# Kernel tuning notes

Measured on AMD Instinct MI355X. Metric: run time of the kernel, lower is better.

## Reference

```python
import jax, jax.numpy as jnp
import numpy as np

B, DIM = 16384, 1024
H1, H2, H3 = 500, 200, 200


def setup_inputs() -> dict:
    key = jax.random.key(0)
    ks = jax.random.split(key, 16)
    s = 0.01
    return {
        "x": jax.random.normal(ks[0], (B, DIM), dtype=jnp.float32),
        "show_index": jax.random.randint(ks[1], (B,), 0, 100),
        "st": jax.random.normal(ks[2], (1000, 16), dtype=jnp.float32),
        # deep MLP params (shared across the two task heads, as in the source)
        "W1": jax.random.normal(ks[3], (DIM, H1), dtype=jnp.float32) * s,
        "b1": jnp.zeros((H1,), dtype=jnp.float32),
        "W2": jax.random.normal(ks[4], (H1, H2), dtype=jnp.float32) * s,
        "b2": jnp.zeros((H2,), dtype=jnp.float32),
        "W3": jax.random.normal(ks[5], (H2, H3), dtype=jnp.float32) * s,
        "b3": jnp.zeros((H3,), dtype=jnp.float32),
        # final sigmoid head on concat([emb(DIM), d3(H3)])
        "Wl": jax.random.normal(ks[6], (DIM + H3, 1), dtype=jnp.float32) * s,
        "bl": jnp.zeros((1,), dtype=jnp.float32),
        # per-(task, cross-layer) cross weights/biases: tf.random_normal stddev=0.01
        "cw": jax.random.normal(ks[7], (2, 3, DIM), dtype=jnp.float32) * s,
        "cb": jax.random.normal(ks[8], (2, 3, DIM), dtype=jnp.float32) * s,
    }


def reference(x, show_index, st, W1, b1, W2, b2, W3, b3, Wl, bl, cw, cb):
    # Deep part (same shared Dense layers each task -> compute once).
    d = jax.nn.relu(x @ W1 + b1)
    d = jax.nn.relu(d @ W2 + b2)
    d3 = jax.nn.relu(d @ W3 + b3)  # (B, H3)

    # cross_net: sum_i w[j] * x[b,i] * emb[b,j]  ==  x.sum(1) * emb[b,j] * w[j]
    # (collapsed form of the (B,dim,dim) outer product + axis-1 reduction)
    xsum = jnp.sum(x, axis=1, keepdims=True)  # (B, 1)
    preds = []
    for i in range(2):
        emb = x
        for j in range(3):
            emb = xsum * emb * cw[i, j] + cb[i, j] + x
        mid = jnp.concatenate([emb, d3], axis=-1)  # (B, DIM+H3)
        preds.append(jax.nn.sigmoid(mid @ Wl + bl))  # (B, 1)
    return tuple(preds)
```

## Files before the change

### kernel.cpp

```cpp
#include <hip/hip_runtime.h>
#include <hip/hip_bf16.h>
#include <math.h>

#define B_ROWS 16384
#define DIM 1024

typedef __attribute__((ext_vector_type(8))) short s16x8;
typedef __attribute__((ext_vector_type(4))) float f32x4;

static __device__ __forceinline__ unsigned short f2bf(float f) {
    union { float f; unsigned u; } v; v.f = f;
    unsigned r = v.u + 0x7FFF + ((v.u >> 16) & 1);
    return (unsigned short)(r >> 16);
}

static __device__ __forceinline__ void gload16(const unsigned short* g, unsigned short* l) {
    __builtin_amdgcn_global_load_lds(
        (const __attribute__((address_space(1))) unsigned int*)g,
        (__attribute__((address_space(3))) unsigned int*)l, 16, 0, 0);
}

__global__ __launch_bounds__(256) void prep(
    const float* __restrict__ x, unsigned short* __restrict__ xb,
    const float* __restrict__ W1, const float* __restrict__ W2,
    const float* __restrict__ W3,
    const float* __restrict__ cw, const float* __restrict__ cb,
    const float* __restrict__ Wl,
    unsigned short* __restrict__ W1b, unsigned short* __restrict__ W2b,
    unsigned short* __restrict__ W3b,
    float* __restrict__ czz) {
    __shared__ unsigned short tile[64][72];
    __shared__ float red[4][6];
    const int tid = threadIdx.x;
    const int blk = blockIdx.x;

    if (blk < 4096) {
        const float* src = x + (size_t)blk * 4096;
        unsigned short* dst = xb + (size_t)blk * 4096;
#pragma unroll
        for (int r = 0; r < 4; ++r) {
            float4 f = *(const float4*)(src + r * 1024 + tid * 4);
            short4 h;
            h.x = (short)f2bf(f.x); h.y = (short)f2bf(f.y);
            h.z = (short)f2bf(f.z); h.w = (short)f2bf(f.w);
            *(short4*)(dst + r * 1024 + tid * 4) = h;
        }
    } else if (blk < 4272) {
        const int w = blk - 4096;
        const float* src; unsigned short* dst;
        int kt, nt, Ksrc, Nsrc, ldDst;
        bool skipHi = false;
        if (w < 128)      { kt = w & 15;         nt = w >> 4;         src = W1; dst = W1b; Ksrc = 1024; Nsrc = 500; ldDst = 1024; skipHi = true; }
        else if (w < 160) { kt = (w - 128) & 7;  nt = (w - 128) >> 3; src = W2; dst = W2b; Ksrc = 500;  Nsrc = 200; ldDst = 512;  }
        else              { kt = (w - 160) & 3;  nt = (w - 160) >> 2; src = W3; dst = W3b; Ksrc = 200;  Nsrc = 200; ldDst = 256;  }
        const int k0 = kt << 6, n0 = nt << 6;
        {
            const int r = tid >> 2, c0 = (tid & 3) << 4;
            const int kk = k0 + r;
#pragma unroll
            for (int i = 0; i < 16; ++i) {
                const int nn = n0 + c0 + i;
                const float v = (kk < Ksrc && nn < Nsrc) ? src[(size_t)kk * Nsrc + nn] : 0.f;
                tile[r][c0 + i] = f2bf(v);
            }
        }
        __syncthreads();
        {
            const int n = tid >> 2, kc = (tid & 3) << 4;
            if (!(skipHi && (n0 + n) >= 500)) {
                unsigned short* o = dst + (size_t)(n0 + n) * ldDst + k0 + kc;
#pragma unroll
                for (int i = 0; i < 16; ++i) o[i] = tile[kc + i][n];
            }
        }
    } else if (blk == 4272) {
#pragma unroll
        for (int q = 0; q < 4; ++q) {
            const int k = tid * 4 + q;
            const float wl = Wl[k];
            const float a1 = cw[k],         a2 = cw[1024 + k],  a3 = cw[2048 + k];
            const float d1_ = cw[3072 + k], d2_ = cw[4096 + k], d3_ = cw[5120 + k];
            W1b[(size_t)500 * 1024 + k] = f2bf(a1 * a2 * a3 * wl);
            W1b[(size_t)501 * 1024 + k] = f2bf(a2 * a3 * wl);
            W1b[(size_t)502 * 1024 + k] = f2bf(a3 * wl);
            W1b[(size_t)503 * 1024 + k] = f2bf(d1_ * d2_ * d3_ * wl);
            W1b[(size_t)504 * 1024 + k] = f2bf(d2_ * d3_ * wl);
            W1b[(size_t)505 * 1024 + k] = f2bf(d3_ * wl);
            W1b[(size_t)506 * 1024 + k] = f2bf(wl);
            W1b[(size_t)507 * 1024 + k] = 0x3F80;
            W1b[(size_t)508 * 1024 + k] = 0;
            W1b[(size_t)509 * 1024 + k] = 0;
            W1b[(size_t)510 * 1024 + k] = 0;
            W1b[(size_t)511 * 1024 + k] = 0;
        }
    } else {
        float c[6] = {0.f, 0.f, 0.f, 0.f, 0.f, 0.f};
#pragma unroll
        for (int q = 0; q < 4; ++q) {
            const int k = tid * 4 + q;
            const float wl = Wl[k];
            {
                const float w2 = cw[1024 + k], w3 = cw[2048 + k];
                const float b1 = cb[k], b2 = cb[1024 + k], b3 = cb[2048 + k];
                c[0] += w2 * w3 * b1 * wl;
                c[1] += w3 * b2 * wl;
                c[2] += b3 * wl;
            }
            {
                const float w2 = cw[4096 + k], w3 = cw[5120 + k];
                const float b1 = cb[3072 + k], b2 = cb[4096 + k], b3 = cb[5120 + k];
                c[3] += w2 * w3 * b1 * wl;
                c[4] += w3 * b2 * wl;
                c[5] += b3 * wl;
            }
        }
        const int lane = tid & 63, wv = tid >> 6;
#pragma unroll
        for (int j = 0; j < 6; ++j)
#pragma unroll
            for (int m = 1; m < 64; m <<= 1) c[j] += __shfl_xor(c[j], m, 64);
        if (lane == 0)
#pragma unroll
            for (int j = 0; j < 6; ++j) red[wv][j] = c[j];
        __syncthreads();
        if (tid < 6) czz[tid] = red[0][tid] + red[1][tid] + red[2][tid] + red[3][tid];
    }
}

template <int ROWS>
static __device__ __forceinline__ void stage_tile(
    const unsigned short* __restrict__ src, int K, int rowBase, int kt,
    unsigned short* lds, int w, int lane) {
    const int r8   = lane >> 3;
    const int slot = lane & 7;
#pragma unroll
    for (int q = 0; q < ROWS / 32; ++q) {
        const int blk   = q * 4 + w;
        const int row   = blk * 8 + r8;
        const int chunk = slot ^ (row & 7);
        const unsigned short* g = src + (size_t)(rowBase + row) * K + kt * 64 + chunk * 8;
        gload16(g, lds + blk * 512);
    }
}

template <int ROWS>
static __device__ __forceinline__ void stage8(
    const unsigned short* __restrict__ src, int K, int rowBase, int kt,
    unsigned short* lds, int w, int lane) {
    const int r8   = lane >> 3;
    const int slot = lane & 7;
#pragma unroll
    for (int q = 0; q < ROWS / 64; ++q) {
        const int blk   = q * 8 + w;
        const int row   = blk * 8 + r8;
        const int chunk = slot ^ (row & 7);
        const unsigned short* g = src + (size_t)(rowBase + row) * K + kt * 64 + chunk * 8;
        gload16(g, lds + blk * 512);
    }
}

__global__ __launch_bounds__(256) void gemm_bf16(
    const unsigned short* __restrict__ A,
    const unsigned short* __restrict__ Bw,
    const float* __restrict__ bias,
    unsigned short* __restrict__ C,
    float* __restrict__ zparts) {
    constexpr int K = 1024, ldc = 512, BM = 128, nK = 16;
    __shared__ unsigned short As[2][BM * 64];
    __shared__ unsigned short Bs[2][128 * 64];

    const int tid  = threadIdx.x;
    const int lane = tid & 63;
    const int wid  = tid >> 6;
    const int wm   = wid >> 1;
    const int wn   = wid & 1;
    const int g    = lane >> 4;
    const int r16  = lane & 15;

    const int cpx = gridDim.x >> 3;
    const int swz = (blockIdx.x & 7) * cpx + (blockIdx.x >> 3);
    const int rowBase = (swz >> 2) * BM;
    const int colBase = (swz & 3) << 7;

    f32x4 acc[4][4];
#pragma unroll
    for (int m = 0; m < 4; ++m)
#pragma unroll
        for (int n = 0; n < 4; ++n)
            acc[m][n] = (f32x4){0.f, 0.f, 0.f, 0.f};

    stage_tile<BM>(A, K, rowBase, 0, As[0], wid, lane);
    stage_tile<128>(Bw, K, colBase, 0, Bs[0], wid, lane);
    asm volatile("s_waitcnt vmcnt(0)" ::: "memory");
    __builtin_amdgcn_s_barrier();
    asm volatile("" ::: "memory");

    for (int kt = 0; kt < nK; ++kt) {
        const int buf = kt & 1;
        if (kt + 1 < nK) {
            stage_tile<BM>(A, K, rowBase, kt + 1, As[buf ^ 1], wid, lane);
            stage_tile<128>(Bw, K, colBase, kt + 1, Bs[buf ^ 1], wid, lane);
        }
        asm volatile("" ::: "memory");

        const unsigned short* Ab = As[buf];
        const unsigned short* Bb = Bs[buf];
#pragma unroll
        for (int ks = 0; ks < 2; ++ks) {
            s16x8 af[4], bfr[4];
#pragma unroll
            for (int m = 0; m < 4; ++m) {
                const int row = wm * 64 + m * 16 + r16;
                const int off = ((ks * 4 + g) * 16) ^ ((row & 7) << 4);
                af[m] = *(const s16x8*)((const char*)Ab + row * 128 + off);
            }
#pragma unroll
            for (int n = 0; n < 4; ++n) {
                const int row = wn * 64 + n * 16 + r16;
                const int off = ((ks * 4 + g) * 16) ^ ((row & 7) << 4);
                bfr[n] = *(const s16x8*)((const char*)Bb + row * 128 + off);
            }
#pragma unroll
            for (int m = 0; m < 4; ++m)
#pragma unroll
                for (int n = 0; n < 4; ++n)
                    acc[m][n] = __builtin_amdgcn_mfma_f32_16x16x32_bf16(af[m], bfr[n], acc[m][n], 0, 0, 0);
        }

        if (kt + 1 < nK)
            asm volatile("s_waitcnt vmcnt(0)" ::: "memory");
        __builtin_amdgcn_s_barrier();
        asm volatile("" ::: "memory");
    }

    unsigned short* Cb = As[0];
#pragma unroll
    for (int n = 0; n < 4; ++n) {
        const int col = colBase + wn * 64 + n * 16 + r16;
        const int lcol = wn * 64 + n * 16 + r16;
        const float bv = (col < 500) ? bias[col] : 0.f;
        const unsigned pc = (unsigned)(col - 500);
#pragma unroll
        for (int m = 0; m < 4; ++m) {
            const int lrow = wm * 64 + m * 16 + g * 4;
#pragma unroll
            for (int r = 0; r < 4; ++r) {
                const float raw = acc[m][n][r];
                if (pc < 8u) zparts[(size_t)(rowBase + lrow + r) * 8 + pc] = raw;
                float v = raw + bv;
                v = v > 0.f ? v : 0.f;
                Cb[(lrow + r) * 128 + lcol] = f2bf(v);
            }
        }
    }
    __syncthreads();

    {
        const int row  = tid >> 1;
        const int half = tid & 1;
        const uint4* s = (const uint4*)(Cb + row * 128 + half * 64);
        uint4* d = (uint4*)(C + (size_t)(rowBase + row) * ldc + colBase + half * 64);
        d[0] = s[0];
        d[1] = s[1];
        d[2] = s[2];
        d[3] = s[3];
    }
}

__global__ __launch_bounds__(512) void tail_fused(
    const unsigned short* __restrict__ d1,
    const unsigned short* __restrict__ W2b,
    const float* __restrict__ b2,
    const unsigned short* __restrict__ W3b,
    const float* __restrict__ b3,
    const float* __restrict__ Wl,
    const float* __restrict__ bl,
    const float* __restrict__ zparts,
    const float* __restrict__ czz,
    float* __restrict__ out) {
    __shared__ unsigned short As[2][64 * 64];
    __shared__ unsigned short Bs[2][256 * 64];
    __shared__ unsigned short P[64 * 256];
    __shared__ float part[8][64];

    const int tid  = threadIdx.x;
    const int lane = tid & 63;
    const int wid  = tid >> 6;
    const int wm   = wid >> 2;
    const int wn   = wid & 3;
    const int g    = lane >> 4;
    const int r16  = lane & 15;
    const int rowBase = blockIdx.x << 6;

    f32x4 acc[2][4];
#pragma unroll
    for (int m = 0; m < 2; ++m)
#pragma unroll
        for (int n = 0; n < 4; ++n)
            acc[m][n] = (f32x4){0.f, 0.f, 0.f, 0.f};

    stage8<64>(d1, 512, rowBase, 0, As[0], wid, lane);
    stage8<256>(W2b, 512, 0, 0, Bs[0], wid, lane);

    for (int kt = 0; kt < 8; ++kt) {
        const int buf = kt & 1;
        if (kt + 1 < 8) {
            stage8<64>(d1, 512, rowBase, kt + 1, As[buf ^ 1], wid, lane);
            stage8<256>(W2b, 512, 0, kt + 1, Bs[buf ^ 1], wid, lane);
            asm volatile("s_waitcnt vmcnt(5)" ::: "memory");
        } else {
            asm volatile("s_waitcnt vmcnt(0)" ::: "memory");
        }
        __builtin_amdgcn_s_barrier();
        asm volatile("" ::: "memory");

        const unsigned short* Ab = As[buf];
        const unsigned short* Bb = Bs[buf];
#pragma unroll
        for (int ks = 0; ks < 2; ++ks) {
            s16x8 af[2], bfr[4];
#pragma unroll
            for (int m = 0; m < 2; ++m) {
                const int row = wm * 32 + m * 16 + r16;
                const int off = ((ks * 4 + g) * 16) ^ ((row & 7) << 4);
                af[m] = *(const s16x8*)((const char*)Ab + row * 128 + off);
            }
#pragma unroll
            for (int n = 0; n < 4; ++n) {
                const int row = wn * 64 + n * 16 + r16;
                const int off = ((ks * 4 + g) * 16) ^ ((row & 7) << 4);
                bfr[n] = *(const s16x8*)((const char*)Bb + row * 128 + off);
            }
#pragma unroll
            for (int m = 0; m < 2; ++m)
#pragma unroll
                for (int n = 0; n < 4; ++n)
                    acc[m][n] = __builtin_amdgcn_mfma_f32_16x16x32_bf16(af[m], bfr[n], acc[m][n], 0, 0, 0);
        }
        asm volatile("s_waitcnt lgkmcnt(0)" ::: "memory");
        __builtin_amdgcn_s_barrier();
        asm volatile("" ::: "memory");
    }

#pragma unroll
    for (int n = 0; n < 4; ++n) {
        const int col = wn * 64 + n * 16 + r16;
        const float bv = (col < 200) ? b2[col] : 0.f;
#pragma unroll
        for (int m = 0; m < 2; ++m) {
#pragma unroll
            for (int r = 0; r < 4; ++r) {
                const int row = wm * 32 + m * 16 + g * 4 + r;
                float v = acc[m][n][r] + bv;
                v = v > 0.f ? v : 0.f;
                const int byte = row * 512 + ((col * 2) ^ ((row & 7) << 4));
                *(unsigned short*)((char*)P + byte) = f2bf(v);
            }
        }
    }

    stage8<256>(W3b, 256, 0, 0, Bs[0], wid, lane);
    asm volatile("s_waitcnt lgkmcnt(0)" ::: "memory");
    __builtin_amdgcn_s_barrier();
    asm volatile("" ::: "memory");

    f32x4 acc2[2][4];
#pragma unroll
    for (int m = 0; m < 2; ++m)
#pragma unroll
        for (int n = 0; n < 4; ++n)
            acc2[m][n] = (f32x4){0.f, 0.f, 0.f, 0.f};

    for (int kt = 0; kt < 4; ++kt) {
        const int buf = kt & 1;
        if (kt + 1 < 4) {
            stage8<256>(W3b, 256, 0, kt + 1, Bs[buf ^ 1], wid, lane);
            asm volatile("s_waitcnt vmcnt(4)" ::: "memory");
        } else {
            asm volatile("s_waitcnt vmcnt(0)" ::: "memory");
        }
        __builtin_amdgcn_s_barrier();
        asm volatile("" ::: "memory");

        const unsigned short* Bb = Bs[buf];
#pragma unroll
        for (int ks = 0; ks < 2; ++ks) {
            s16x8 af[2], bfr[4];
#pragma unroll
            for (int m = 0; m < 2; ++m) {
                const int row = wm * 32 + m * 16 + r16;
                const int byte = row * 512 + ((kt * 128 + (ks * 4 + g) * 16) ^ ((row & 7) << 4));
                af[m] = *(const s16x8*)((const char*)P + byte);
            }
#pragma unroll
            for (int n = 0; n < 4; ++n) {
                const int row = wn * 64 + n * 16 + r16;
                const int off = ((ks * 4 + g) * 16) ^ ((row & 7) << 4);
                bfr[n] = *(const s16x8*)((const char*)Bb + row * 128 + off);
            }
#pragma unroll
            for (int m = 0; m < 2; ++m)
#pragma unroll
                for (int n = 0; n < 4; ++n)
                    acc2[m][n] = __builtin_amdgcn_mfma_f32_16x16x32_bf16(af[m], bfr[n], acc2[m][n], 0, 0, 0);
        }
        asm volatile("s_waitcnt lgkmcnt(0)" ::: "memory");
        __builtin_amdgcn_s_barrier();
        asm volatile("" ::: "memory");
    }

    float wlv[4], b3v[4];
#pragma unroll
    for (int n = 0; n < 4; ++n) {
        const int col = wn * 64 + n * 16 + r16;
        wlv[n] = (col < 200) ? Wl[1024 + col] : 0.f;
        b3v[n] = (col < 200) ? b3[col] : 0.f;
    }
#pragma unroll
    for (int m = 0; m < 2; ++m) {
#pragma unroll
        for (int r = 0; r < 4; ++r) {
            float s = 0.f;
#pragma unroll
            for (int n = 0; n < 4; ++n) {
                float v = acc2[m][n][r] + b3v[n];
                v = v > 0.f ? v : 0.f;
                s += v * wlv[n];
            }
            s += __shfl_xor(s, 1, 64);
            s += __shfl_xor(s, 2, 64);
            s += __shfl_xor(s, 4, 64);
            s += __shfl_xor(s, 8, 64);
            if (r16 == 0) part[wid][wm * 32 + m * 16 + g * 4 + r] = s;
        }
    }
    __syncthreads();

    if (tid < 64) {
        const int row = rowBase + tid;
        const int wmr = (tid >> 5) << 2;
        const float t = part[wmr][tid] + part[wmr + 1][tid] +
                        part[wmr + 2][tid] + part[wmr + 3][tid];
        const float blv = bl[0];
        const float* zp = zparts + (size_t)row * 8;
        float4 zpa = *(const float4*)(zp);
        float4 zpb = *(const float4*)(zp + 4);
        const float s = zpb.w;
        const float z0 = ((zpa.x * s + zpa.y + czz[0]) * s + zpa.z + czz[1]) * s
                         + zpb.z + czz[2] + t + blv;
        const float z1 = ((zpa.w * s + zpb.x + czz[3]) * s + zpb.y + czz[4]) * s
                         + zpb.z + czz[5] + t + blv;
        out[row]          = 1.f / (1.f + expf(-z0));
        out[B_ROWS + row] = 1.f / (1.f + expf(-z1));
    }
}

extern "C" void kernel_launch(void* const* d_in, const int* in_sizes, int n_in,
                              void* d_out, int out_size, void* d_ws, size_t ws_size,
                              hipStream_t stream) {
    const float* x  = (const float*)d_in[0];
    const float* W1 = (const float*)d_in[3];
    const float* b1 = (const float*)d_in[4];
    const float* W2 = (const float*)d_in[5];
    const float* b2 = (const float*)d_in[6];
    const float* W3 = (const float*)d_in[7];
    const float* b3 = (const float*)d_in[8];
    const float* Wl = (const float*)d_in[9];
    const float* bl = (const float*)d_in[10];
    const float* cw = (const float*)d_in[11];
    const float* cb = (const float*)d_in[12];
    float* out = (float*)d_out;

    unsigned short* xb  = (unsigned short*)d_ws;
    unsigned short* d1  = xb + (size_t)16384 * 1024;
    unsigned short* W1b = d1 + (size_t)16384 * 512;
    unsigned short* W2b = W1b + (size_t)512 * 1024;
    unsigned short* W3b = W2b + (size_t)256 * 512;
    float* zparts = (float*)(W3b + (size_t)256 * 256);
    float* czz = zparts + (size_t)16384 * 8;

    prep<<<4274, 256, 0, stream>>>(x, xb, W1, W2, W3, cw, cb, Wl,
                                   W1b, W2b, W3b, czz);

    gemm_bf16<<<512, 256, 0, stream>>>(xb, W1b, b1, d1, zparts);

    tail_fused<<<256, 512, 0, stream>>>(d1, W2b, b2, W3b, b3, Wl, bl,
                                        zparts, czz, out);
}
```

Measured before the change: 61.46 us.

## Switch first-layer GEMM to FP8 and compute cross-net dot products in FP32

Quantizes x and W1 to FP8 (E4M3, with W1 scaled by 64) and runs the first GEMM with FP8 MFMA instructions over 128-byte K tiles. The cross-net per-row dot products move from extra W1 rows inside the GEMM to a separate FP32 kernel, which also writes the FP8 copy of x. The goal is to halve GEMM operand bytes and raise MFMA throughput. The cost is lower precision in the deep path and one extra kernel launch.

```diff
diff --git a/kernel.cpp b/kernel.cpp
--- a/kernel.cpp
+++ b/kernel.cpp
@@ -14,45 +14,44 @@
     return (unsigned short)(r >> 16);
 }
 
-static __device__ __forceinline__ void gload16(const unsigned short* g, unsigned short* l) {
+static __device__ __forceinline__ unsigned f2fp8(float f) {
+    union { float f; unsigned u; } v; v.f = f;
+    const unsigned s = (v.u >> 24) & 0x80u;
+    const float a = fabsf(f);
+    if (a >= 448.f) return s | 0x7Eu;
+    if (a < 0.015625f) {
+        const int q = (int)rintf(a * 512.f);
+        return s | (unsigned)q;
+    }
+    unsigned b = v.u & 0x7fffffffu;
+    b += 0x000FFFFFu + ((b >> 20) & 1u);
+    const int e = (int)(b >> 23) - 127;
+    const unsigned m = (b >> 20) & 7u;
+    return s | (unsigned)((e + 7) << 3) | m;
+}
+
+static __device__ __forceinline__ void gload16(const void* g, void* l) {
     __builtin_amdgcn_global_load_lds(
         (const __attribute__((address_space(1))) unsigned int*)g,
         (__attribute__((address_space(3))) unsigned int*)l, 16, 0, 0);
 }
 
-__global__ __launch_bounds__(256) void prep(
-    const float* __restrict__ x, unsigned short* __restrict__ xb,
+__global__ __launch_bounds__(256) void prep_w(
     const float* __restrict__ W1, const float* __restrict__ W2,
     const float* __restrict__ W3,
     const float* __restrict__ cw, const float* __restrict__ cb,
     const float* __restrict__ Wl,
-    unsigned short* __restrict__ W1b, unsigned short* __restrict__ W2b,
-    unsigned short* __restrict__ W3b,
+    unsigned char* __restrict__ W1q,
+    unsigned short* __restrict__ W2b, unsigned short* __restrict__ W3b,
     float* __restrict__ czz) {
     __shared__ unsigned short tile[64][72];
+    __shared__ unsigned char tilec[64][72];
     __shared__ float red[4][6];
     const int tid = threadIdx.x;
     const int blk = blockIdx.x;
 
-    if (blk < 4096) {
-        const float* src = x + (size_t)blk * 4096;
-        unsigned short* dst = xb + (size_t)blk * 4096;
-#pragma unroll
-        for (int r = 0; r < 4; ++r) {
-            float4 f = *(const float4*)(src + r * 1024 + tid * 4);
-            short4 h;
-            h.x = (short)f2bf(f.x); h.y = (short)f2bf(f.y);
-            h.z = (short)f2bf(f.z); h.w = (short)f2bf(f.w);
-            *(short4*)(dst + r * 1024 + tid * 4) = h;
-        }
-    } else if (blk < 4272) {
-        const int w = blk - 4096;
-        const float* src; unsigned short* dst;
-        int kt, nt, Ksrc, Nsrc, ldDst;
-        bool skipHi = false;
-        if (w < 128)      { kt = w & 15;         nt = w >> 4;         src = W1; dst = W1b; Ksrc = 1024; Nsrc = 500; ldDst = 1024; skipHi = true; }
-        else if (w < 160) { kt = (w - 128) & 7;  nt = (w - 128) >> 3; src = W2; dst = W2b; Ksrc = 500;  Nsrc = 200; ldDst = 512;  }
-        else              { kt = (w - 160) & 3;  nt = (w - 160) >> 2; src = W3; dst = W3b; Ksrc = 200;  Nsrc = 200; ldDst = 256;  }
+    if (blk < 128) {
+        const int kt = blk & 15, nt = blk >> 4;
         const int k0 = kt << 6, n0 = nt << 6;
         {
             const int r = tid >> 2, c0 = (tid & 3) << 4;
@@ -60,38 +59,40 @@
 #pragma unroll
             for (int i = 0; i < 16; ++i) {
                 const int nn = n0 + c0 + i;
-                const float v = (kk < Ksrc && nn < Nsrc) ? src[(size_t)kk * Nsrc + nn] : 0.f;
-                tile[r][c0 + i] = f2bf(v);
+                const float v = (nn < 500) ? W1[(size_t)kk * 500 + nn] * 64.f : 0.f;
+                tilec[r][c0 + i] = (unsigned char)f2fp8(v);
             }
         }
         __syncthreads();
         {
             const int n = tid >> 2, kc = (tid & 3) << 4;
-            if (!(skipHi && (n0 + n) >= 500)) {
-                unsigned short* o = dst + (size_t)(n0 + n) * ldDst + k0 + kc;
-#pragma unroll
-                for (int i = 0; i < 16; ++i) o[i] = tile[kc + i][n];
-            }
-        }
-    } else if (blk == 4272) {
-#pragma unroll
-        for (int q = 0; q < 4; ++q) {
-            const int k = tid * 4 + q;
-            const float wl = Wl[k];
-            const float a1 = cw[k],         a2 = cw[1024 + k],  a3 = cw[2048 + k];
-            const float d1_ = cw[3072 + k], d2_ = cw[4096 + k], d3_ = cw[5120 + k];
-            W1b[(size_t)500 * 1024 + k] = f2bf(a1 * a2 * a3 * wl);
-            W1b[(size_t)501 * 1024 + k] = f2bf(a2 * a3 * wl);
-            W1b[(size_t)502 * 1024 + k] = f2bf(a3 * wl);
-            W1b[(size_t)503 * 1024 + k] = f2bf(d1_ * d2_ * d3_ * wl);
-            W1b[(size_t)504 * 1024 + k] = f2bf(d2_ * d3_ * wl);
-            W1b[(size_t)505 * 1024 + k] = f2bf(d3_ * wl);
-            W1b[(size_t)506 * 1024 + k] = f2bf(wl);
-            W1b[(size_t)507 * 1024 + k] = 0x3F80;
-            W1b[(size_t)508 * 1024 + k] = 0;
-            W1b[(size_t)509 * 1024 + k] = 0;
-            W1b[(size_t)510 * 1024 + k] = 0;
-            W1b[(size_t)511 * 1024 + k] = 0;
+            unsigned char* o = W1q + (size_t)(n0 + n) * 1024 + k0 + kc;
+#pragma unroll
+            for (int i = 0; i < 16; ++i) o[i] = tilec[kc + i][n];
+        }
+    } else if (blk < 176) {
+        const int w = blk;
+        const float* src; unsigned short* dst;
+        int kt, nt, Ksrc, Nsrc, ldDst;
+        if (w < 160) { kt = (w - 128) & 7;  nt = (w - 128) >> 3; src = W2; dst = W2b; Ksrc = 500; Nsrc = 200; ldDst = 512; }
+        else         { kt = (w - 160) & 3;  nt = (w - 160) >> 2; src = W3; dst = W3b; Ksrc = 200; Nsrc = 200; ldDst = 256; }
+        const int k0 = kt << 6, n0 = nt << 6;
+        {
+            const int r = tid >> 2, c0 = (tid & 3) << 4;
+            const int kk = k0 + r;
+#pragma unroll
+            for (int i = 0; i < 16; ++i) {
+                const int nn = n0 + c0 + i;
+                const float v = (kk < Ksrc && nn < Nsrc) ? src[(size_t)kk * Nsrc + nn] : 0.f;
+                tile[r][c0 + i] = f2bf(v);
+            }
+        }
+        __syncthreads();
+        {
+            const int n = tid >> 2, kc = (tid & 3) << 4;
+            unsigned short* o = dst + (size_t)(n0 + n) * ldDst + k0 + kc;
+#pragma unroll
+            for (int i = 0; i < 16; ++i) o[i] = tile[kc + i][n];
         }
     } else {
         float c[6] = {0.f, 0.f, 0.f, 0.f, 0.f, 0.f};
@@ -127,47 +128,97 @@
     }
 }
 
-template <int ROWS>
-static __device__ __forceinline__ void stage_tile(
-    const unsigned short* __restrict__ src, int K, int rowBase, int kt,
-    unsigned short* lds, int w, int lane) {
+__global__ __launch_bounds__(256) void xdots(
+    const float* __restrict__ x,
+    const float* __restrict__ cw, const float* __restrict__ Wl,
+    unsigned char* __restrict__ xq,
+    float* __restrict__ zparts) {
+    const int tid  = threadIdx.x;
+    const int lane = tid & 63;
+    const int w    = tid >> 6;
+    const int row0 = (blockIdx.x << 4) + (w << 2);
+
+    float d[4][8];
+#pragma unroll
+    for (int r = 0; r < 4; ++r)
+#pragma unroll
+        for (int j = 0; j < 8; ++j) d[r][j] = 0.f;
+
+#pragma unroll
+    for (int c = 0; c < 4; ++c) {
+        const int kb = c * 256 + lane * 4;
+        const float4 wl4 = *(const float4*)(Wl + kb);
+        const float4 c0 = *(const float4*)(cw + kb);
+        const float4 c1 = *(const float4*)(cw + 1024 + kb);
+        const float4 c2 = *(const float4*)(cw + 2048 + kb);
+        const float4 c3 = *(const float4*)(cw + 3072 + kb);
+        const float4 c4 = *(const float4*)(cw + 4096 + kb);
+        const float4 c5 = *(const float4*)(cw + 5120 + kb);
+        float4 p10, p20, p30, p11, p21, p31;
+        p10.x = c2.x * wl4.x; p10.y = c2.y * wl4.y; p10.z = c2.z * wl4.z; p10.w = c2.w * wl4.w;
+        p20.x = c1.x * p10.x; p20.y = c1.y * p10.y; p20.z = c1.z * p10.z; p20.w = c1.w * p10.w;
+        p30.x = c0.x * p20.x; p30.y = c0.y * p20.y; p30.z = c0.z * p20.z; p30.w = c0.w * p20.w;
+        p11.x = c5.x * wl4.x; p11.y = c5.y * wl4.y; p11.z = c5.z * wl4.z; p11.w = c5.w * wl4.w;
+        p21.x = c4.x * p11.x; p21.y = c4.y * p11.y; p21.z = c4.z * p11.z; p21.w = c4.w * p11.w;
+        p31.x = c3.x * p21.x; p31.y = c3.y * p21.y; p31.z = c3.z * p21.z; p31.w = c3.w * p21.w;
+
+#pragma unroll
+        for (int r = 0; r < 4; ++r) {
+            const float4 xv = *(const float4*)(x + (size_t)(row0 + r) * DIM + kb);
+            d[r][0] += xv.x * p30.x + xv.y * p30.y + xv.z * p30.z + xv.w * p30.w;
+            d[r][1] += xv.x * p20.x + xv.y * p20.y + xv.z * p20.z + xv.w * p20.w;
+            d[r][2] += xv.x * p10.x + xv.y * p10.y + xv.z * p10.z + xv.w * p10.w;
+            d[r][3] += xv.x * p31.x + xv.y * p31.y + xv.z * p31.z + xv.w * p31.w;
+            d[r][4] += xv.x * p21.x + xv.y * p21.y + xv.z * p21.z + xv.w * p21.w;
+            d[r][5] += xv.x * p11.x + xv.y * p11.y + xv.z * p11.z + xv.w * p11.w;
+            d[r][6] += xv.x * wl4.x + xv.y * wl4.y + xv.z * wl4.z + xv.w * wl4.w;
+            d[r][7] += xv.x + xv.y + xv.z + xv.w;
+            const unsigned u = f2fp8(xv.x) | (f2fp8(xv.y) << 8) |
+                               (f2fp8(xv.z) << 16) | (f2fp8(xv.w) << 24);
+            *(unsigned*)(xq + (size_t)(row0 + r) * DIM + kb) = u;
+        }
+    }
+
+#pragma unroll
+    for (int r = 0; r < 4; ++r)
+#pragma unroll
+        for (int j = 0; j < 8; ++j)
+#pragma unroll
+            for (int m = 1; m < 64; m <<= 1)
+                d[r][j] += __shfl_xor(d[r][j], m, 64);
+
+    if (lane == 0) {
+#pragma unroll
+        for (int r = 0; r < 4; ++r)
+#pragma unroll
+            for (int j = 0; j < 8; ++j)
+                zparts[(size_t)(row0 + r) * 8 + j] = d[r][j];
+    }
+}
+
+static __device__ __forceinline__ void stage_fp8(
+    const unsigned char* __restrict__ src, int rowBase, int kt,
+    unsigned char* lds, int w, int lane) {
     const int r8   = lane >> 3;
     const int slot = lane & 7;
 #pragma unroll
-    for (int q = 0; q < ROWS / 32; ++q) {
+    for (int q = 0; q < 4; ++q) {
         const int blk   = q * 4 + w;
         const int row   = blk * 8 + r8;
         const int chunk = slot ^ (row & 7);
-        const unsigned short* g = src + (size_t)(rowBase + row) * K + kt * 64 + chunk * 8;
-        gload16(g, lds + blk * 512);
-    }
-}
-
-template <int ROWS>
-static __device__ __forceinline__ void stage8(
-    const unsigned short* __restrict__ src, int K, int rowBase, int kt,
-    unsigned short* lds, int w, int lane) {
-    const int r8   = lane >> 3;
-    const int slot = lane & 7;
-#pragma unroll
-    for (int q = 0; q < ROWS / 64; ++q) {
-        const int blk   = q * 8 + w;
-        const int row   = blk * 8 + r8;
-        const int chunk = slot ^ (row & 7);
-        const unsigned short* g = src + (size_t)(rowBase + row) * K + kt * 64 + chunk * 8;
-        gload16(g, lds + blk * 512);
-    }
-}
-
-__global__ __launch_bounds__(256) void gemm_bf16(
-    const unsigned short* __restrict__ A,
-    const unsigned short* __restrict__ Bw,
+        gload16(src + (size_t)(rowBase + row) * 1024 + kt * 128 + chunk * 16,
+                lds + blk * 1024);
+    }
+}
+
+__global__ __launch_bounds__(256) void gemm_fp8(
+    const unsigned char* __restrict__ A,
+    const unsigned char* __restrict__ Bq,
     const float* __restrict__ bias,
-    unsigned short* __restrict__ C,
-    float* __restrict__ zparts) {
-    constexpr int K = 1024, ldc = 512, BM = 128, nK = 16;
-    __shared__ unsigned short As[2][BM * 64];
-    __shared__ unsigned short Bs[2][128 * 64];
+    unsigned short* __restrict__ C) {
+    constexpr int nK = 8;
+    __shared__ unsigned char As[2][128 * 128];
+    __shared__ unsigned char Bs[2][128 * 128];
 
     const int tid  = threadIdx.x;
     const int lane = tid & 63;
@@ -179,7 +230,7 @@
 
     const int cpx = gridDim.x >> 3;
     const int swz = (blockIdx.x & 7) * cpx + (blockIdx.x >> 3);
-    const int rowBase = (swz >> 2) * BM;
+    const int rowBase = (swz >> 2) << 7;
     const int colBase = (swz & 3) << 7;
 
     f32x4 acc[4][4];
@@ -189,8 +240,8 @@
         for (int n = 0; n < 4; ++n)
             acc[m][n] = (f32x4){0.f, 0.f, 0.f, 0.f};
 
-    stage_tile<BM>(A, K, rowBase, 0, As[0], wid, lane);
-    stage_tile<128>(Bw, K, colBase, 0, Bs[0], wid, lane);
+    stage_fp8(A, rowBase, 0, As[0], wid, lane);
+    stage_fp8(Bq, colBase, 0, Bs[0], wid, lane);
     asm volatile("s_waitcnt vmcnt(0)" ::: "memory");
     __builtin_amdgcn_s_barrier();
     asm volatile("" ::: "memory");
@@ -198,56 +249,55 @@
     for (int kt = 0; kt < nK; ++kt) {
         const int buf = kt & 1;
         if (kt + 1 < nK) {
-            stage_tile<BM>(A, K, rowBase, kt + 1, As[buf ^ 1], wid, lane);
-            stage_tile<128>(Bw, K, colBase, kt + 1, Bs[buf ^ 1], wid, lane);
+            stage_fp8(A, rowBase, kt + 1, As[buf ^ 1], wid, lane);
+            stage_fp8(Bq, colBase, kt + 1, Bs[buf ^ 1], wid, lane);
         }
         asm volatile("" ::: "memory");
 
-        const unsigned short* Ab = As[buf];
-        const unsigned short* Bb = Bs[buf];
-#pragma unroll
-        for (int ks = 0; ks < 2; ++ks) {
-            s16x8 af[4], bfr[4];
+        const unsigned char* Ab = As[buf];
+        const unsigned char* Bb = Bs[buf];
+#pragma unroll
+        for (int ks = 0; ks < 4; ++ks) {
+            long af[4], bf[4];
 #pragma unroll
             for (int m = 0; m < 4; ++m) {
                 const int row = wm * 64 + m * 16 + r16;
-                const int off = ((ks * 4 + g) * 16) ^ ((row & 7) << 4);
-                af[m] = *(const s16x8*)((const char*)Ab + row * 128 + off);
+                const int byte = row * 128 +
+                    ((((ks << 1) | (g >> 1)) ^ (row & 7)) << 4) + ((g & 1) << 3);
+                af[m] = *(const long*)(Ab + byte);
             }
 #pragma unroll
             for (int n = 0; n < 4; ++n) {
                 const int row = wn * 64 + n * 16 + r16;
-                const int off = ((ks * 4 + g) * 16) ^ ((row & 7) << 4);
-                bfr[n] = *(const s16x8*)((const char*)Bb + row * 128 + off);
+                const int byte = row * 128 +
+                    ((((ks << 1) | (g >> 1)) ^ (row & 7)) << 4) + ((g & 1) << 3);
+                bf[n] = *(const long*)(Bb + byte);
             }
 #pragma unroll
             for (int m = 0; m < 4; ++m)
 #pragma unroll
                 for (int n = 0; n < 4; ++n)
-                    acc[m][n] = __builtin_amdgcn_mfma_f32_16x16x32_bf16(af[m], bfr[n], acc[m][n], 0, 0, 0);
-        }
-
-        if (kt + 1 < nK)
-            asm volatile("s_waitcnt vmcnt(0)" ::: "memory");
+                    acc[m][n] = __builtin_amdgcn_mfma_f32_16x16x32_fp8_fp8(
+                        af[m], bf[n], acc[m][n], 0, 0, 0);
+        }
+
+        asm volatile("s_waitcnt vmcnt(0)" ::: "memory");
         __builtin_amdgcn_s_barrier();
         asm volatile("" ::: "memory");
     }
 
-    unsigned short* Cb = As[0];
+    unsigned short* Cb = (unsigned short*)As[0];
 #pragma unroll
     for (int n = 0; n < 4; ++n) {
-        const int col = colBase + wn * 64 + n * 16 + r16;
         const int lcol = wn * 64 + n * 16 + r16;
+        const int col = colBase + lcol;
         const float bv = (col < 500) ? bias[col] : 0.f;
-        const unsigned pc = (unsigned)(col - 500);
 #pragma unroll
         for (int m = 0; m < 4; ++m) {
             const int lrow = wm * 64 + m * 16 + g * 4;
 #pragma unroll
             for (int r = 0; r < 4; ++r) {
-                const float raw = acc[m][n][r];
-                if (pc < 8u) zparts[(size_t)(rowBase + lrow + r) * 8 + pc] = raw;
-                float v = raw + bv;
+                float v = acc[m][n][r] * 0.015625f + bv;
                 v = v > 0.f ? v : 0.f;
                 Cb[(lrow + r) * 128 + lcol] = f2bf(v);
             }
@@ -259,24 +309,33 @@
         const int row  = tid >> 1;
         const int half = tid & 1;
         const uint4* s = (const uint4*)(Cb + row * 128 + half * 64);
-        uint4* d = (uint4*)(C + (size_t)(rowBase + row) * ldc + colBase + half * 64);
-        d[0] = s[0];
-        d[1] = s[1];
-        d[2] = s[2];
-        d[3] = s[3];
+        uint4* dd = (uint4*)(C + (size_t)(rowBase + row) * 512 + colBase + half * 64);
+        dd[0] = s[0]; dd[1] = s[1]; dd[2] = s[2]; dd[3] = s[3];
+    }
+}
+
+template <int ROWS>
+static __device__ __forceinline__ void stage8(
+    const unsigned short* __restrict__ src, int K, int rowBase, int kt,
+    unsigned short* lds, int w, int lane) {
+    const int r8   = lane >> 3;
+    const int slot = lane & 7;
+#pragma unroll
+    for (int q = 0; q < ROWS / 64; ++q) {
+        const int blk   = q * 8 + w;
+        const int row   = blk * 8 + r8;
+        const int chunk = slot ^ (row & 7);
+        gload16(src + (size_t)(rowBase + row) * K + kt * 64 + chunk * 8,
+                lds + blk * 512);
     }
 }
 
 __global__ __launch_bounds__(512) void tail_fused(
     const unsigned short* __restrict__ d1,
-    const unsigned short* __restrict__ W2b,
-    const float* __restrict__ b2,
-    const unsigned short* __restrict__ W3b,
-    const float* __restrict__ b3,
-    const float* __restrict__ Wl,
-    const float* __restrict__ bl,
-    const float* __restrict__ zparts,
-    const float* __restrict__ czz,
+    const unsigned short* __restrict__ W2b, const float* __restrict__ b2,
+    const unsigned short* __restrict__ W3b, const float* __restrict__ b3,
+    const float* __restrict__ Wl, const float* __restrict__ bl,
+    const float* __restrict__ zparts, const float* __restrict__ czz,
     float* __restrict__ out) {
     __shared__ unsigned short As[2][64 * 64];
     __shared__ unsigned short Bs[2][256 * 64];
@@ -471,18 +530,19 @@
     const float* cb = (const float*)d_in[12];
     float* out = (float*)d_out;
 
-    unsigned short* xb  = (unsigned short*)d_ws;
-    unsigned short* d1  = xb + (size_t)16384 * 1024;
-    unsigned short* W1b = d1 + (size_t)16384 * 512;
-    unsigned short* W2b = W1b + (size_t)512 * 1024;
+    unsigned short* d1  = (unsigned short*)d_ws;
+    unsigned char*  xq  = (unsigned char*)(d1 + (size_t)16384 * 512);
+    unsigned char*  W1q = xq + (size_t)16384 * 1024;
+    unsigned short* W2b = (unsigned short*)(W1q + (size_t)512 * 1024);
     unsigned short* W3b = W2b + (size_t)256 * 512;
     float* zparts = (float*)(W3b + (size_t)256 * 256);
     float* czz = zparts + (size_t)16384 * 8;
 
-    prep<<<4274, 256, 0, stream>>>(x, xb, W1, W2, W3, cw, cb, Wl,
-                                   W1b, W2b, W3b, czz);
-
-    gemm_bf16<<<512, 256, 0, stream>>>(xb, W1b, b1, d1, zparts);
+    prep_w<<<177, 256, 0, stream>>>(W1, W2, W3, cw, cb, Wl, W1q, W2b, W3b, czz);
+
+    xdots<<<1024, 256, 0, stream>>>(x, cw, Wl, xq, zparts);
+
+    gemm_fp8<<<512, 256, 0, stream>>>(xq, W1q, b1, d1);
 
     tail_fused<<<256, 512, 0, stream>>>(d1, W2b, b2, W3b, b3, Wl, bl,
                                         zparts, czz, out);
```

Measured after the change: 72.99 us. 1.19x slower.
